# Kernel tuning notes

Measured on AMD Instinct MI355X. Metric: run time of the kernel, lower is better.

## Reference

```python
import jax, jax.numpy as jnp
from jax import lax
import numpy as np

K = 4            # prototypes per class: 3 kmeans centroids + 1 backbone
EPS = 0.1        # sinkhorn entropic regularization
MAX_ITER = 100
THRESH = 0.01
KM_ITERS = 10    # Lloyd iterations (replaces host-side sklearn KMeans)
HW = 28          # the original reshapes pred to 28x28, fixing n = 784


def setup_inputs():
    key = jax.random.key(0)
    k1, k2, k3, k4 = jax.random.split(key, 4)
    b, n, d, c = 32, HW * HW, 1024, 20
    return {
        "query": jax.random.normal(k1, (b, n, d), dtype=jnp.float32),
        "score": jax.random.uniform(k2, (b, n, c), dtype=jnp.float32),
        "label": jax.random.randint(k3, (b, c), 0, 2),
        "gt": jax.random.randint(k4, (b, HW, HW), 0, c + 1),
        "weights": jnp.array([1.0, 1.0, 0.0, -1.0], dtype=jnp.float32),
    }


def _assign(dq, cen, selfm):
    # dq [b,m,d], cen [b,c,j,d], selfm [b,c,m] float mask -> one-hot labels, counts
    x2 = jnp.sum(dq * dq, axis=-1)                                   # [b,m]
    d2 = (x2[:, None, :, None]
          - 2.0 * jnp.einsum('bmd,bcjd->bcmj', dq, cen)
          + jnp.sum(cen * cen, axis=-1)[:, :, None, :])              # [b,c,m,j]
    oh = jax.nn.one_hot(jnp.argmin(d2, axis=-1), cen.shape[2], dtype=dq.dtype) * selfm[..., None]
    return oh, oh.sum(axis=2)


def _sinkhorn(Km, u, v):
    # vectorized over the [b,c] pair grid, per-pair early exit as in the torch loop
    def cond(st):
        it, r, cc, done = st
        return (it < MAX_ITER) & jnp.logical_not(jnp.all(done))

    def body(st):
        it, r, cc, done = st
        r1 = u / jnp.einsum('bcnj,bcj->bcn', Km, cc)
        c1 = v / jnp.einsum('bcnj,bcn->bcj', Km, r1)
        err = jnp.mean(jnp.abs(r1 - r), axis=-1)                     # [b,c]
        r = jnp.where(done[..., None], r, r1)
        cc = jnp.where(done[..., None], cc, c1)
        done = done | (err < THRESH)
        return it + 1, r, cc, done

    st = (jnp.int32(0), jnp.ones_like(u), jnp.ones_like(v),
          jnp.zeros(Km.shape[:2], dtype=bool))
    _, r, cc, _ = lax.while_loop(cond, body, st)
    return r[..., :, None] * cc[..., None, :] * Km                   # [b,c,n,K]


def _forward(query, score, label, gt, weights):
    b, n, d = query.shape
    c = score.shape[2]
    dq, ds = query[:, ::2, :], score[:, ::2, :]                      # stride-2 downsample
    m = dq.shape[1]
    cls_assign = jnp.argmax(ds, axis=-1)                             # [b,m]
    sel = cls_assign[:, None, :] == jnp.arange(c)[None, :, None]     # [b,c,m]
    selfm = sel.astype(query.dtype)
    cnt = selfm.sum(-1)                                              # [b,c]
    valid = (label > 0) & (cnt >= K)

    # ---- masked Lloyd's k-means with k-1 = 3 clusters per (image, class) pair
    order = jnp.argsort((~sel).astype(jnp.int32), axis=-1)           # masked points first
    init_idx = order[..., :K - 1]                                    # [b,c,3]
    cen = dq[jnp.arange(b)[:, None, None], init_idx]                 # [b,c,3,d]

    def km_step(cen, _):
        oh, kcnt = _assign(dq, cen, selfm)
        sums = jnp.einsum('bmd,bcmj->bcjd', dq, oh)
        cen = jnp.where(kcnt[..., None] > 0,
                        sums / jnp.maximum(kcnt, 1.0)[..., None], cen)
        return cen, None

    cen, _ = lax.scan(km_step, cen, None, length=KM_ITERS)
    oh, kcnt = _assign(dq, cen, selfm)                               # final labels

    # ---- sort centroids by mean cluster score (descending)
    sm = ds.mean(axis=-1)                                            # [b,m]
    avg = jnp.where(kcnt > 0,
                    jnp.einsum('bm,bcmj->bcj', sm, oh) / jnp.maximum(kcnt, 1.0),
                    -jnp.inf)
    ordj = jnp.argsort(-avg, axis=-1)                                # [b,c,3]
    cen = jnp.take_along_axis(cen, ordj[..., None], axis=2)

    # ---- backbone prototype = mean over unselected downsampled tokens
    un = 1.0 - selfm
    backbone = jnp.einsum('bmd,bcm->bcd', dq, un) / jnp.maximum(m - cnt, 1.0)[..., None]
    protos = jnp.concatenate([cen, backbone[:, :, None, :]], axis=2)  # [b,c,4,d]

    # ---- OT between query[0] tokens and the 4 prototypes (original uses query[0] always)
    q0 = query[0]
    q0h = q0 / jnp.maximum(jnp.linalg.norm(q0, axis=-1, keepdims=True), 1e-12)
    ph = protos / jnp.maximum(jnp.linalg.norm(protos, axis=-1, keepdims=True), 1e-12)
    sim = jnp.einsum('nd,bcjd->bcnj', q0h, ph)                       # [b,c,n,4]
    Km = lax.stop_gradient(jnp.exp(-(1.0 - sim) / EPS))              # torch.no_grad
    u = jnp.full((b, c, n), 1.0 / n, dtype=query.dtype)
    v = jnp.full((b, c, K), 1.0 / K, dtype=query.dtype)
    T = lax.stop_gradient(_sinkhorn(Km, u, v))                       # [b,c,n,4]

    valid = valid & jnp.logical_not(jnp.any(jnp.isnan(T), axis=(2, 3)))
    pred = jnp.einsum('bcnj,j->bcn', T, weights)                     # [b,c,n]

    # ---- BCE vs gt masks (28x28 -> 28x28 bilinear resize is the identity)
    y = (gt.reshape(b, -1)[:, None, :] == (jnp.arange(c) + 1)[None, :, None]).astype(pred.dtype)
    p = jnp.clip(pred, 0.0, 1.0)
    bce = -(y * jnp.maximum(jnp.log(p), -100.0)
            + (1.0 - y) * jnp.maximum(jnp.log(1.0 - p), -100.0)).mean(axis=-1)  # [b,c]
    bce = jnp.where(valid, bce, 0.0)
    total_n = valid.sum().astype(pred.dtype)
    return bce.sum() / (total_n + 1e-4)


def reference(query, score, label, gt, weights):
    return _forward(query, score, label, gt, weights)
```

## Files before the change

kernel.cpp:

```cpp
#include <hip/hip_runtime.h>
#include <cmath>

#define BB 32
#define NN 784
#define MM 392
#define DD 1024
#define CC 20
#define JJ 3
#define KP 4
#define KM_ITERS 10
#define GMAX 64
#define NCOL (BB * CC * KP)
#define NQ0B 98
#define NTSB (BB * 16)

typedef __attribute__((ext_vector_type(8))) short bf16x8;
typedef __attribute__((ext_vector_type(4))) float f32x4;

__device__ inline unsigned short f2bf(float x) {
  unsigned int u = __float_as_uint(x);
  u += 0x7FFFu + ((u >> 16) & 1u);
  return (unsigned short)(u >> 16);
}
__device__ inline float bf2f(unsigned short h) {
  return __uint_as_float(((unsigned int)h) << 16);
}
__device__ inline void f2bf2(float x, unsigned short& hi, unsigned short& lo) {
  hi = f2bf(x);
  lo = f2bf(x - bf2f(hi));
}
__device__ inline void store_bf4(unsigned short* baseh, unsigned short* basel,
                                 int idx4, float4 v) {
  ushort4 h, l;
  f2bf2(v.x, h.x, l.x); f2bf2(v.y, h.y, l.y);
  f2bf2(v.z, h.z, l.z); f2bf2(v.w, h.w, l.w);
  ((ushort4*)baseh)[idx4] = h;
  ((ushort4*)basel)[idx4] = l;
}

__global__ __launch_bounds__(512) void k_prep(
    const float* __restrict__ score, const float* __restrict__ query,
    const int* __restrict__ label,
    int* __restrict__ cls, float* __restrict__ sm, int* __restrict__ valid,
    float* __restrict__ totalsum,
    unsigned short* __restrict__ q0hh, unsigned short* __restrict__ q0hl,
    float* __restrict__ gred) {
  int blk = blockIdx.x;
  int tid = threadIdx.x, lane = tid & 63, wv = tid >> 6;
  __shared__ int s_cnt[CC];
  __shared__ float sa[8][64];

  if (blk < BB) {
    int b = blk;
    if (tid < CC) s_cnt[tid] = 0;
    __syncthreads();
    if (tid < MM) {
      const float4* s4 = (const float4*)(score + ((size_t)b * NN + 2 * tid) * CC);
      float4 r[5];
      #pragma unroll
      for (int k = 0; k < 5; k++) r[k] = s4[k];
      const float* s = (const float*)r;
      float best = s[0]; int bi = 0; float acc = s[0];
      #pragma unroll
      for (int c = 1; c < CC; c++) { float v = s[c]; acc += v; if (v > best) { best = v; bi = c; } }
      cls[b * MM + tid] = bi;
      sm[b * MM + tid] = acc / (float)CC;
      atomicAdd(&s_cnt[bi], 1);
    }
    __syncthreads();
    if (tid < CC) {
      int cv = s_cnt[tid];
      valid[b * CC + tid] = (label[b * CC + tid] > 0 && cv >= KP) ? 1 : 0;
    }
    if (blk == 0 && tid == 0) { gred[0] = 0.f; gred[1] = 0.f; ((int*)gred)[2] = 0; }
  } else if (blk < BB + NQ0B) {
    int n = (blk - BB) * 8 + wv;
    const float* src = query + (size_t)n * DD;
    float v[16];
    float ss = 0.f;
    #pragma unroll
    for (int j = 0; j < 16; j++) { v[j] = src[lane + 64 * j]; ss += v[j] * v[j]; }
    #pragma unroll
    for (int o = 32; o > 0; o >>= 1) ss += __shfl_xor(ss, o, 64);
    float nrm = fmaxf(sqrtf(ss), 1e-12f);
    #pragma unroll
    for (int j = 0; j < 16; j++) {
      unsigned short hi, lo;
      f2bf2(v[j] / nrm, hi, lo);
      q0hh[(size_t)n * DD + lane + 64 * j] = hi;
      q0hl[(size_t)n * DD + lane + 64 * j] = lo;
    }
  } else {
    int t = blk - BB - NQ0B;
    int b = t >> 4, ch = t & 15;
    const float* qb = query + (size_t)b * NN * DD + ch * 64 + lane;
    float a = 0.f;
    #pragma unroll 7
    for (int r = 0; r < 49; r++) {
      int i = wv * 49 + r;
      a += qb[(size_t)(2 * i) * DD];
    }
    sa[wv][lane] = a;
    __syncthreads();
    if (wv == 0) {
      float s = 0.f;
      #pragma unroll
      for (int w = 0; w < 8; w++) s += sa[w][lane];
      totalsum[(size_t)b * DD + ch * 64 + lane] = s;
    }
  }
}

__global__ __launch_bounds__(512) void k_gram(
    const float* __restrict__ query, const int* __restrict__ cls,
    const int* __restrict__ valid, const float* __restrict__ sm,
    const float* __restrict__ totalsum,
    unsigned short* __restrict__ phh, unsigned short* __restrict__ phl) {
  int bc = blockIdx.x;
  if (!valid[bc]) return;
  int b = bc / CC, c = bc - b * CC;
  int tid = threadIdx.x, lane = tid & 63, wv = tid >> 6;
  const float* qb = query + (size_t)b * NN * DD;
  __shared__ int s_wtot[8];
  __shared__ int s_list[GMAX];
  __shared__ __align__(16) float Xs[GMAX][132];
  __shared__ float Gl[GMAX][65];
  __shared__ float s_w[JJ][GMAX];
  __shared__ int s_rank[JJ];
  __shared__ float s_red2[8];

  int flag = 0;
  if (tid < MM) flag = (cls[b * MM + tid] == c) ? 1 : 0;
  unsigned long long msk = __ballot(flag);
  int wp = __popcll(msk & ((1ull << lane) - 1ull));
  if (lane == 0) s_wtot[wv] = __popcll(msk);
  __syncthreads();
  int off = 0, mtot = 0;
  #pragma unroll
  for (int w = 0; w < 8; w++) { int t = s_wtot[w]; if (w < wv) off += t; mtot += t; }
  int mc = mtot > GMAX ? GMAX : mtot;
  if (flag) { int pos = off + wp; if (pos < GMAX) s_list[pos] = tid; }
  __syncthreads();

  const float* pb[4] = {nullptr, nullptr, nullptr, nullptr};
  float* xd[4] = {nullptr, nullptr, nullptr, nullptr};
  #pragma unroll
  for (int s = 0; s < 4; s++) {
    int e = tid + s * 512;
    if (e < mc * 32) {
      pb[s] = qb + (size_t)(2 * s_list[e >> 5]) * DD + (e & 31) * 4;
      xd[s] = &Xs[e >> 5][(e & 31) * 4];
    }
  }

  int T = (mc + 3) >> 2;
  int ntile = T * (T + 1) / 2;
  int ti = -1, tj = 0;
  float a[4][4] = {};
  if (tid < ntile) {
    int p = tid;
    int i = (int)floorf((sqrtf(8.0f * (float)p + 1.0f) - 1.0f) * 0.5f);
    while ((i + 1) * (i + 2) / 2 <= p) i++;
    while (i * (i + 1) / 2 > p) i--;
    ti = i; tj = p - i * (i + 1) / 2;
  }

  float4 cur[4], nxt[4];
  #pragma unroll
  for (int s = 0; s < 4; s++) {
    cur[s] = make_float4(0.f, 0.f, 0.f, 0.f);
    nxt[s] = make_float4(0.f, 0.f, 0.f, 0.f);
    if (pb[s]) cur[s] = *(const float4*)(pb[s]);
  }
  for (int ch = 0; ch < 8; ch++) {
    __syncthreads();
    #pragma unroll
    for (int s = 0; s < 4; s++) if (pb[s]) *(float4*)xd[s] = cur[s];
    if (ch < 7) {
      #pragma unroll
      for (int s = 0; s < 4; s++) if (pb[s]) nxt[s] = *(const float4*)(pb[s] + (ch + 1) * 128);
    }
    __syncthreads();
    if (ti >= 0) {
      const float4* xr0 = (const float4*)&Xs[4 * ti + 0][0];
      const float4* xr1 = (const float4*)&Xs[4 * ti + 1][0];
      const float4* xr2 = (const float4*)&Xs[4 * ti + 2][0];
      const float4* xr3 = (const float4*)&Xs[4 * ti + 3][0];
      const float4* xc0 = (const float4*)&Xs[4 * tj + 0][0];
      const float4* xc1 = (const float4*)&Xs[4 * tj + 1][0];
      const float4* xc2 = (const float4*)&Xs[4 * tj + 2][0];
      const float4* xc3 = (const float4*)&Xs[4 * tj + 3][0];
      #pragma unroll 8
      for (int kk = 0; kk < 32; kk++) {
        float4 u[4], w[4];
        u[0] = xr0[kk]; u[1] = xr1[kk]; u[2] = xr2[kk]; u[3] = xr3[kk];
        w[0] = xc0[kk]; w[1] = xc1[kk]; w[2] = xc2[kk]; w[3] = xc3[kk];
        #pragma unroll
        for (int r = 0; r < 4; r++)
          #pragma unroll
          for (int cq = 0; cq < 4; cq++)
            a[r][cq] += u[r].x * w[cq].x + u[r].y * w[cq].y
                      + u[r].z * w[cq].z + u[r].w * w[cq].w;
      }
    }
    #pragma unroll
    for (int s = 0; s < 4; s++) cur[s] = nxt[s];
  }

  if (ti >= 0) {
    #pragma unroll
    for (int r = 0; r < 4; r++) {
      int gr = 4 * ti + r;
      if (gr < mc) {
        #pragma unroll
        for (int cq = 0; cq < 4; cq++) {
          int gc = 4 * tj + cq;
          if (gc < mc) { Gl[gr][gc] = a[r][cq]; Gl[gc][gr] = a[r][cq]; }
        }
      }
    }
  }
  __syncthreads();

  if (wv == 0) {
    bool act = lane < mc;
    float smv = act ? sm[b * MM + s_list[lane]] : 0.f;
    s_w[0][lane] = (lane == 0) ? 1.f : 0.f;
    s_w[1][lane] = (lane == 1) ? 1.f : 0.f;
    s_w[2][lane] = (lane == 2) ? 1.f : 0.f;
    int aj = 0, n0 = 0, n1 = 0, n2 = 0;
    for (int it = 0; it <= KM_ITERS; it++) {
      float h0 = 0.f, h1 = 0.f, h2 = 0.f;
      if (act) {
        for (int i = 0; i < mc; i++) {
          float g = Gl[lane][i];
          h0 += s_w[0][i] * g; h1 += s_w[1][i] * g; h2 += s_w[2][i] * g;
        }
      }
      float t0 = s_w[0][lane] * h0, t1 = s_w[1][lane] * h1, t2 = s_w[2][lane] * h2;
      for (int o = 1; o < 64; o <<= 1) {
        t0 += __shfl_xor(t0, o, 64); t1 += __shfl_xor(t1, o, 64); t2 += __shfl_xor(t2, o, 64);
      }
      float e0 = t0 - 2.f * h0, e1 = t1 - 2.f * h1, e2 = t2 - 2.f * h2;
      aj = 0; float bv = e0;
      if (e1 < bv) { bv = e1; aj = 1; }
      if (e2 < bv) { bv = e2; aj = 2; }
      n0 = __popcll(__ballot(act && aj == 0));
      n1 = __popcll(__ballot(act && aj == 1));
      n2 = __popcll(__ballot(act && aj == 2));
      if (it == KM_ITERS) break;
      if (act) {
        if (n0 > 0) s_w[0][lane] = (aj == 0) ? 1.f / (float)n0 : 0.f;
        if (n1 > 0) s_w[1][lane] = (aj == 1) ? 1.f / (float)n1 : 0.f;
        if (n2 > 0) s_w[2][lane] = (aj == 2) ? 1.f / (float)n2 : 0.f;
      }
    }
    float s0 = (act && aj == 0) ? smv : 0.f;
    float s1 = (act && aj == 1) ? smv : 0.f;
    float s2 = (act && aj == 2) ? smv : 0.f;
    for (int o = 1; o < 64; o <<= 1) {
      s0 += __shfl_xor(s0, o, 64); s1 += __shfl_xor(s1, o, 64); s2 += __shfl_xor(s2, o, 64);
    }
    if (lane == 0) {
      float avg[JJ];
      avg[0] = (n0 > 0) ? s0 / (float)n0 : -INFINITY;
      avg[1] = (n1 > 0) ? s1 / (float)n1 : -INFINITY;
      avg[2] = (n2 > 0) ? s2 / (float)n2 : -INFINITY;
      bool used[JJ] = {false, false, false};
      for (int s = 0; s < JJ; s++) {
        int bi = -1; float bv = 0.f;
        for (int j = 0; j < JJ; j++)
          if (!used[j] && (bi < 0 || avg[j] > bv)) { bi = j; bv = avg[j]; }
        used[bi] = true; s_rank[bi] = s;
      }
    }
  }
  __syncthreads();

  float4 a0 = make_float4(0.f, 0.f, 0.f, 0.f), a1 = make_float4(0.f, 0.f, 0.f, 0.f);
  int j = tid >> 7, q = tid & 127;
  if (j < 3) {
    for (int g = 0; g < mc; g++) {
      float w = s_w[j][g];
      if (w != 0.f) {
        const float4* row = (const float4*)(qb + (size_t)(2 * s_list[g]) * DD);
        float4 v0 = row[q], v1 = row[q + 128];
        a0.x += w * v0.x; a0.y += w * v0.y; a0.z += w * v0.z; a0.w += w * v0.w;
        a1.x += w * v1.x; a1.y += w * v1.y; a1.z += w * v1.z; a1.w += w * v1.w;
      }
    }
  } else {
    for (int g = 0; g < mc; g++) {
      const float4* row = (const float4*)(qb + (size_t)(2 * s_list[g]) * DD);
      float4 v0 = row[q], v1 = row[q + 128];
      a0.x += v0.x; a0.y += v0.y; a0.z += v0.z; a0.w += v0.w;
      a1.x += v1.x; a1.y += v1.y; a1.z += v1.z; a1.w += v1.w;
    }
    const float4* tb = (const float4*)(totalsum + (size_t)b * DD);
    float4 t0 = tb[q], t1 = tb[q + 128];
    float denom = fmaxf((float)(MM - mtot), 1.f);
    float inv = 1.f / denom;
    a0.x = (t0.x - a0.x) * inv; a0.y = (t0.y - a0.y) * inv;
    a0.z = (t0.z - a0.z) * inv; a0.w = (t0.w - a0.w) * inv;
    a1.x = (t1.x - a1.x) * inv; a1.y = (t1.y - a1.y) * inv;
    a1.z = (t1.z - a1.z) * inv; a1.w = (t1.w - a1.w) * inv;
  }
  float ssq = a0.x * a0.x + a0.y * a0.y + a0.z * a0.z + a0.w * a0.w
            + a1.x * a1.x + a1.y * a1.y + a1.z * a1.z + a1.w * a1.w;
  #pragma unroll
  for (int o = 1; o < 64; o <<= 1) ssq += __shfl_xor(ssq, o, 64);
  if (lane == 0) s_red2[wv] = ssq;
  __syncthreads();
  float nrm = fmaxf(sqrtf(s_red2[2 * j] + s_red2[2 * j + 1]), 1e-12f);
  int prow = (j < 3) ? s_rank[j] : 3;
  size_t rowoff = ((size_t)bc * KP + prow) * DD;
  float4 o0 = make_float4(a0.x / nrm, a0.y / nrm, a0.z / nrm, a0.w / nrm);
  float4 o1 = make_float4(a1.x / nrm, a1.y / nrm, a1.z / nrm, a1.w / nrm);
  store_bf4(phh + rowoff, phl + rowoff, q, o0);
  store_bf4(phh + rowoff, phl + rowoff, q + 128, o1);
}

__global__ __launch_bounds__(64) void k_gemm(
    const unsigned short* __restrict__ Ah, const unsigned short* __restrict__ Al,
    const unsigned short* __restrict__ Bh, const unsigned short* __restrict__ Bl,
    float* __restrict__ P) {
  int n0 = blockIdx.y * 64;
  int m0 = blockIdx.x * 64;
  int lane = threadIdx.x;
  int kh = lane >> 4;
  int lr = lane & 15;

  const unsigned short* pa_h[4]; const unsigned short* pa_l[4];
  #pragma unroll
  for (int mi = 0; mi < 4; mi++) {
    size_t o = (size_t)(m0 + mi * 16 + lr) * DD + kh * 8;
    pa_h[mi] = Ah + o; pa_l[mi] = Al + o;
  }
  const unsigned short* pb_h[4]; const unsigned short* pb_l[4];
  #pragma unroll
  for (int ni = 0; ni < 4; ni++) {
    int col = n0 + ni * 16 + lr;
    size_t o = (size_t)col * DD + kh * 8;
    pb_h[ni] = Bh + o; pb_l[ni] = Bl + o;
  }

  f32x4 acc[4][4];
  #pragma unroll
  for (int mi = 0; mi < 4; mi++)
    #pragma unroll
    for (int ni = 0; ni < 4; ni++) acc[mi][ni] = (f32x4){0.f, 0.f, 0.f, 0.f};

  for (int k0 = 0; k0 < DD; k0 += 32) {
    bf16x8 ah[4], al[4], bh[4], bl[4];
    #pragma unroll
    for (int i = 0; i < 4; i++) {
      ah[i] = *(const bf16x8*)(pa_h[i] + k0);
      al[i] = *(const bf16x8*)(pa_l[i] + k0);
      bh[i] = *(const bf16x8*)(pb_h[i] + k0);
      bl[i] = *(const bf16x8*)(pb_l[i] + k0);
    }
    #pragma unroll
    for (int mi = 0; mi < 4; mi++)
      #pragma unroll
      for (int ni = 0; ni < 4; ni++) {
        acc[mi][ni] = __builtin_amdgcn_mfma_f32_16x16x32_bf16(ah[mi], bh[ni], acc[mi][ni], 0, 0, 0);
        acc[mi][ni] = __builtin_amdgcn_mfma_f32_16x16x32_bf16(ah[mi], bl[ni], acc[mi][ni], 0, 0, 0);
        acc[mi][ni] = __builtin_amdgcn_mfma_f32_16x16x32_bf16(al[mi], bh[ni], acc[mi][ni], 0, 0, 0);
      }
  }

  #pragma unroll
  for (int ni = 0; ni < 4; ni++) {
    int col = n0 + ni * 16 + lr;
    #pragma unroll
    for (int mi = 0; mi < 4; mi++) {
      int m = m0 + mi * 16 + kh * 4;
      if (m < NN) {
        *(f32x4*)(P + (size_t)col * NN + m) = acc[mi][ni];
      }
    }
  }
}

__global__ __launch_bounds__(256) void k_sink(const float* __restrict__ P,
    const int* __restrict__ valid, const int* __restrict__ gt,
    const float* __restrict__ wts, float* __restrict__ gred, float* __restrict__ out) {
  int wv = threadIdx.x >> 6, lane = threadIdx.x & 63;
  int bc = blockIdx.x * 4 + wv;
  int b = bc / CC, c = bc - b * CC;
  float bce_out = 0.f; int vld_out = 0;

  if (valid[bc]) {
    float4 kv[13]; float rr[13];
    #pragma unroll
    for (int s = 0; s < 13; s++) {
      int n = lane + 64 * s;
      kv[s] = make_float4(0.f, 0.f, 0.f, 0.f); rr[s] = 1.f;
      if (n < NN) {
        float4 o;
        o.x = expf(-(1.0f - P[((size_t)(4 * bc + 0)) * NN + n]) / 0.1f);
        o.y = expf(-(1.0f - P[((size_t)(4 * bc + 1)) * NN + n]) / 0.1f);
        o.z = expf(-(1.0f - P[((size_t)(4 * bc + 2)) * NN + n]) / 0.1f);
        o.w = expf(-(1.0f - P[((size_t)(4 * bc + 3)) * NN + n]) / 0.1f);
        kv[s] = o;
      }
    }
    const float uu = 1.0f / (float)NN, vv = 1.0f / (float)KP;
    float c0 = 1.f, c1 = 1.f, c2 = 1.f, c3 = 1.f;
    for (int it = 0; it < 100; it++) {
      float dsum = 0.f, p0 = 0.f, p1 = 0.f, p2 = 0.f, p3 = 0.f;
      #pragma unroll
      for (int s = 0; s < 13; s++) {
        int n = lane + 64 * s;
        if (n < NN) {
          float4 k4 = kv[s];
          float S = k4.x * c0 + k4.y * c1 + k4.z * c2 + k4.w * c3;
          float r1 = uu / S;
          dsum += fabsf(r1 - rr[s]);
          rr[s] = r1;
          p0 += k4.x * r1; p1 += k4.y * r1; p2 += k4.z * r1; p3 += k4.w * r1;
        }
      }
      #pragma unroll
      for (int o = 1; o < 64; o <<= 1) {
        dsum += __shfl_xor(dsum, o, 64);
        p0 += __shfl_xor(p0, o, 64); p1 += __shfl_xor(p1, o, 64);
        p2 += __shfl_xor(p2, o, 64); p3 += __shfl_xor(p3, o, 64);
      }
      c0 = vv / p0; c1 = vv / p1; c2 = vv / p2; c3 = vv / p3;
      if (dsum / (float)NN < 0.01f) break;
    }
    float w0 = wts[0], w1 = wts[1], w2 = wts[2], w3 = wts[3];
    float bsum = 0.f; int nanloc = 0;
    const int* gtb = gt + b * NN;
    #pragma unroll
    for (int s = 0; s < 13; s++) {
      int n = lane + 64 * s;
      if (n < NN) {
        float4 k4 = kv[s];
        float rv = rr[s];
        float T0 = rv * c0 * k4.x, T1 = rv * c1 * k4.y, T2 = rv * c2 * k4.z, T3 = rv * c3 * k4.w;
        if (T0 != T0 || T1 != T1 || T2 != T2 || T3 != T3) nanloc = 1;
        float pred = T0 * w0 + T1 * w1 + T2 * w2 + T3 * w3;
        float pcl = fminf(fmaxf(pred, 0.f), 1.f);
        float t = (gtb[n] == c + 1) ? fmaxf(logf(pcl), -100.f) : fmaxf(logf(1.f - pcl), -100.f);
        bsum += t;
      }
    }
    #pragma unroll
    for (int o = 1; o < 64; o <<= 1) bsum += __shfl_xor(bsum, o, 64);
    int nanany = __any(nanloc);
    if (!nanany) { bce_out = -(bsum / (float)NN); vld_out = 1; }
  }

  if (lane == 0) {
    if (vld_out) { atomicAdd(&gred[0], bce_out); atomicAdd(&gred[1], 1.f); }
    __threadfence();
    int old = atomicAdd((int*)gred + 2, 1);
    if (old == BB * CC - 1) {
      float s = atomicAdd(&gred[0], 0.f);
      float n2 = atomicAdd(&gred[1], 0.f);
      out[0] = s / (n2 + 0.0001f);
    }
  }
}

extern "C" void kernel_launch(void* const* d_in, const int* in_sizes, int n_in,
                              void* d_out, int out_size, void* d_ws, size_t ws_size,
                              hipStream_t stream) {
  (void)in_sizes; (void)n_in; (void)out_size; (void)ws_size;
  const float* query = (const float*)d_in[0];
  const float* score = (const float*)d_in[1];
  const int*   label = (const int*)d_in[2];
  const int*   gt    = (const int*)d_in[3];
  const float* wts   = (const float*)d_in[4];
  float* ws = (float*)d_ws;

  size_t off = 0;
  int* cls = (int*)(ws + off);            off += (size_t)BB * MM;
  float* sm = ws + off;                   off += (size_t)BB * MM;
  int* valid = (int*)(ws + off);          off += (size_t)BB * CC;
  float* totalsum = ws + off;             off += (size_t)BB * DD;
  unsigned short* q0hh = (unsigned short*)(ws + off);  off += (size_t)NN * DD / 2;
  unsigned short* q0hl = (unsigned short*)(ws + off);  off += (size_t)NN * DD / 2;
  unsigned short* phh = (unsigned short*)(ws + off);   off += (size_t)BB * CC * KP * DD / 2;
  unsigned short* phl = (unsigned short*)(ws + off);   off += (size_t)BB * CC * KP * DD / 2;
  float* P = ws + off;                    off += (size_t)NCOL * NN;
  float* gred = ws + off;                 off += 16;

  k_prep<<<BB + NQ0B + NTSB, 512, 0, stream>>>(score, query, label, cls, sm, valid,
                                               totalsum, q0hh, q0hl, gred);
  k_gram<<<BB * CC, 512, 0, stream>>>(query, cls, valid, sm, totalsum, phh, phl);
  dim3 gg((NN + 63) / 64, NCOL / 64);
  k_gemm<<<gg, 64, 0, stream>>>(q0hh, q0hl, phh, phl, P);
  k_sink<<<160, 256, 0, stream>>>(P, valid, gt, wts, gred, (float*)d_out);
}
```

Before: 309.8 us.

## Fuse similarity GEMM into Sinkhorn kernel and retile Gram computation to 2x2

Merges the bf16-split MFMA similarity GEMM into the Sinkhorn kernel. Each 256-thread block computes its 16 prototype columns over all 784 query rows into shared memory, then runs Sinkhorn straight from LDS, which removes the global P buffer round trip and one kernel launch. Separately, the Gram kernel switches from 4x4 to 2x2 register tiles with up to two tiles per thread, trading register pressure for more parallel tiles. The fused GEMM uses single 16x16 MFMA tiles per wave with no operand reuse across tiles, so it reloads the query operand from global memory in every block.

```diff
diff --git a/kernel.cpp b/kernel.cpp
--- a/kernel.cpp
+++ b/kernel.cpp
@@ -153,16 +153,21 @@
     }
   }
 
-  int T = (mc + 3) >> 2;
+  int T = (mc + 1) >> 1;
   int ntile = T * (T + 1) / 2;
-  int ti = -1, tj = 0;
-  float a[4][4] = {};
-  if (tid < ntile) {
-    int p = tid;
-    int i = (int)floorf((sqrtf(8.0f * (float)p + 1.0f) - 1.0f) * 0.5f);
-    while ((i + 1) * (i + 2) / 2 <= p) i++;
-    while (i * (i + 1) / 2 > p) i--;
-    ti = i; tj = p - i * (i + 1) / 2;
+  int ti_[2], tj_[2];
+  float a00[2], a01[2], a10[2], a11[2];
+  #pragma unroll
+  for (int s = 0; s < 2; s++) {
+    ti_[s] = -1; tj_[s] = 0;
+    a00[s] = 0.f; a01[s] = 0.f; a10[s] = 0.f; a11[s] = 0.f;
+    int p = tid + s * 512;
+    if (p < ntile) {
+      int i = (int)floorf((sqrtf(8.0f * (float)p + 1.0f) - 1.0f) * 0.5f);
+      while ((i + 1) * (i + 2) / 2 <= p) i++;
+      while (i * (i + 1) / 2 > p) i--;
+      ti_[s] = i; tj_[s] = p - i * (i + 1) / 2;
+    }
   }
 
   float4 cur[4], nxt[4];
@@ -181,43 +186,37 @@
       for (int s = 0; s < 4; s++) if (pb[s]) nxt[s] = *(const float4*)(pb[s] + (ch + 1) * 128);
     }
     __syncthreads();
-    if (ti >= 0) {
-      const float4* xr0 = (const float4*)&Xs[4 * ti + 0][0];
-      const float4* xr1 = (const float4*)&Xs[4 * ti + 1][0];
-      const float4* xr2 = (const float4*)&Xs[4 * ti + 2][0];
-      const float4* xr3 = (const float4*)&Xs[4 * ti + 3][0];
-      const float4* xc0 = (const float4*)&Xs[4 * tj + 0][0];
-      const float4* xc1 = (const float4*)&Xs[4 * tj + 1][0];
-      const float4* xc2 = (const float4*)&Xs[4 * tj + 2][0];
-      const float4* xc3 = (const float4*)&Xs[4 * tj + 3][0];
-      #pragma unroll 8
-      for (int kk = 0; kk < 32; kk++) {
-        float4 u[4], w[4];
-        u[0] = xr0[kk]; u[1] = xr1[kk]; u[2] = xr2[kk]; u[3] = xr3[kk];
-        w[0] = xc0[kk]; w[1] = xc1[kk]; w[2] = xc2[kk]; w[3] = xc3[kk];
+    #pragma unroll
+    for (int s = 0; s < 2; s++) {
+      if (ti_[s] >= 0) {
+        const float4* xr0 = (const float4*)&Xs[2 * ti_[s]][0];
+        const float4* xr1 = (const float4*)&Xs[2 * ti_[s] + 1][0];
+        const float4* xc0 = (const float4*)&Xs[2 * tj_[s]][0];
+        const float4* xc1 = (const float4*)&Xs[2 * tj_[s] + 1][0];
+        float s00 = 0.f, s01 = 0.f, s10 = 0.f, s11 = 0.f;
         #pragma unroll
-        for (int r = 0; r < 4; r++)
-          #pragma unroll
-          for (int cq = 0; cq < 4; cq++)
-            a[r][cq] += u[r].x * w[cq].x + u[r].y * w[cq].y
-                      + u[r].z * w[cq].z + u[r].w * w[cq].w;
+        for (int kk = 0; kk < 32; kk++) {
+          float4 u0 = xr0[kk], u1 = xr1[kk], w0 = xc0[kk], w1 = xc1[kk];
+          s00 += u0.x * w0.x + u0.y * w0.y + u0.z * w0.z + u0.w * w0.w;
+          s01 += u0.x * w1.x + u0.y * w1.y + u0.z * w1.z + u0.w * w1.w;
+          s10 += u1.x * w0.x + u1.y * w0.y + u1.z * w0.z + u1.w * w0.w;
+          s11 += u1.x * w1.x + u1.y * w1.y + u1.z * w1.z + u1.w * w1.w;
+        }
+        a00[s] += s00; a01[s] += s01; a10[s] += s10; a11[s] += s11;
       }
     }
     #pragma unroll
     for (int s = 0; s < 4; s++) cur[s] = nxt[s];
   }
 
-  if (ti >= 0) {
-    #pragma unroll
-    for (int r = 0; r < 4; r++) {
-      int gr = 4 * ti + r;
-      if (gr < mc) {
-        #pragma unroll
-        for (int cq = 0; cq < 4; cq++) {
-          int gc = 4 * tj + cq;
-          if (gc < mc) { Gl[gr][gc] = a[r][cq]; Gl[gc][gr] = a[r][cq]; }
-        }
-      }
+  #pragma unroll
+  for (int s = 0; s < 2; s++) {
+    if (ti_[s] >= 0) {
+      int r0 = 2 * ti_[s], r1 = r0 + 1, c0 = 2 * tj_[s], c1 = c0 + 1;
+      if (r0 < mc && c0 < mc) { Gl[r0][c0] = a00[s]; Gl[c0][r0] = a00[s]; }
+      if (r0 < mc && c1 < mc) { Gl[r0][c1] = a01[s]; Gl[c1][r0] = a01[s]; }
+      if (r1 < mc && c0 < mc) { Gl[r1][c0] = a10[s]; Gl[c0][r1] = a10[s]; }
+      if (r1 < mc && c1 < mc) { Gl[r1][c1] = a11[s]; Gl[c1][r1] = a11[s]; }
     }
   }
   __syncthreads();
@@ -320,72 +319,37 @@
   store_bf4(phh + rowoff, phl + rowoff, q + 128, o1);
 }
 
-__global__ __launch_bounds__(64) void k_gemm(
+__global__ __launch_bounds__(256) void k_gs(
     const unsigned short* __restrict__ Ah, const unsigned short* __restrict__ Al,
     const unsigned short* __restrict__ Bh, const unsigned short* __restrict__ Bl,
-    float* __restrict__ P) {
-  int n0 = blockIdx.y * 64;
-  int m0 = blockIdx.x * 64;
-  int lane = threadIdx.x;
-  int kh = lane >> 4;
-  int lr = lane & 15;
-
-  const unsigned short* pa_h[4]; const unsigned short* pa_l[4];
-  #pragma unroll
-  for (int mi = 0; mi < 4; mi++) {
-    size_t o = (size_t)(m0 + mi * 16 + lr) * DD + kh * 8;
-    pa_h[mi] = Ah + o; pa_l[mi] = Al + o;
-  }
-  const unsigned short* pb_h[4]; const unsigned short* pb_l[4];
-  #pragma unroll
-  for (int ni = 0; ni < 4; ni++) {
-    int col = n0 + ni * 16 + lr;
-    size_t o = (size_t)col * DD + kh * 8;
-    pb_h[ni] = Bh + o; pb_l[ni] = Bl + o;
-  }
-
-  f32x4 acc[4][4];
-  #pragma unroll
-  for (int mi = 0; mi < 4; mi++)
-    #pragma unroll
-    for (int ni = 0; ni < 4; ni++) acc[mi][ni] = (f32x4){0.f, 0.f, 0.f, 0.f};
-
-  for (int k0 = 0; k0 < DD; k0 += 32) {
-    bf16x8 ah[4], al[4], bh[4], bl[4];
-    #pragma unroll
-    for (int i = 0; i < 4; i++) {
-      ah[i] = *(const bf16x8*)(pa_h[i] + k0);
-      al[i] = *(const bf16x8*)(pa_l[i] + k0);
-      bh[i] = *(const bf16x8*)(pb_h[i] + k0);
-      bl[i] = *(const bf16x8*)(pb_l[i] + k0);
-    }
-    #pragma unroll
-    for (int mi = 0; mi < 4; mi++)
-      #pragma unroll
-      for (int ni = 0; ni < 4; ni++) {
-        acc[mi][ni] = __builtin_amdgcn_mfma_f32_16x16x32_bf16(ah[mi], bh[ni], acc[mi][ni], 0, 0, 0);
-        acc[mi][ni] = __builtin_amdgcn_mfma_f32_16x16x32_bf16(ah[mi], bl[ni], acc[mi][ni], 0, 0, 0);
-        acc[mi][ni] = __builtin_amdgcn_mfma_f32_16x16x32_bf16(al[mi], bh[ni], acc[mi][ni], 0, 0, 0);
-      }
-  }
-
-  #pragma unroll
-  for (int ni = 0; ni < 4; ni++) {
-    int col = n0 + ni * 16 + lr;
-    #pragma unroll
-    for (int mi = 0; mi < 4; mi++) {
-      int m = m0 + mi * 16 + kh * 4;
-      if (m < NN) {
-        *(f32x4*)(P + (size_t)col * NN + m) = acc[mi][ni];
-      }
-    }
-  }
-}
-
-__global__ __launch_bounds__(256) void k_sink(const float* __restrict__ P,
     const int* __restrict__ valid, const int* __restrict__ gt,
     const float* __restrict__ wts, float* __restrict__ gred, float* __restrict__ out) {
-  int wv = threadIdx.x >> 6, lane = threadIdx.x & 63;
+  __shared__ float s_P[NN][17];
+  int tid = threadIdx.x, lane = tid & 63, wv = tid >> 6;
+  int col0 = blockIdx.x * 16;
+  int lr = lane & 15, kh = lane >> 4;
+
+  const unsigned short* pbh = Bh + (size_t)(col0 + lr) * DD + kh * 8;
+  const unsigned short* pbl = Bl + (size_t)(col0 + lr) * DD + kh * 8;
+  for (int mt = wv; mt < 49; mt += 4) {
+    const unsigned short* pah = Ah + (size_t)(mt * 16 + lr) * DD + kh * 8;
+    const unsigned short* pal = Al + (size_t)(mt * 16 + lr) * DD + kh * 8;
+    f32x4 acc = (f32x4){0.f, 0.f, 0.f, 0.f};
+    for (int k0 = 0; k0 < DD; k0 += 32) {
+      bf16x8 fah = *(const bf16x8*)(pah + k0);
+      bf16x8 fal = *(const bf16x8*)(pal + k0);
+      bf16x8 fbh = *(const bf16x8*)(pbh + k0);
+      bf16x8 fbl = *(const bf16x8*)(pbl + k0);
+      acc = __builtin_amdgcn_mfma_f32_16x16x32_bf16(fah, fbh, acc, 0, 0, 0);
+      acc = __builtin_amdgcn_mfma_f32_16x16x32_bf16(fah, fbl, acc, 0, 0, 0);
+      acc = __builtin_amdgcn_mfma_f32_16x16x32_bf16(fal, fbh, acc, 0, 0, 0);
+    }
+    #pragma unroll
+    for (int r = 0; r < 4; r++)
+      s_P[mt * 16 + kh * 4 + r][lr] = acc[r];
+  }
+  __syncthreads();
+
   int bc = blockIdx.x * 4 + wv;
   int b = bc / CC, c = bc - b * CC;
   float bce_out = 0.f; int vld_out = 0;
@@ -397,11 +361,12 @@
       int n = lane + 64 * s;
       kv[s] = make_float4(0.f, 0.f, 0.f, 0.f); rr[s] = 1.f;
       if (n < NN) {
+        int cb = (wv << 2);
         float4 o;
-        o.x = expf(-(1.0f - P[((size_t)(4 * bc + 0)) * NN + n]) / 0.1f);
-        o.y = expf(-(1.0f - P[((size_t)(4 * bc + 1)) * NN + n]) / 0.1f);
-        o.z = expf(-(1.0f - P[((size_t)(4 * bc + 2)) * NN + n]) / 0.1f);
-        o.w = expf(-(1.0f - P[((size_t)(4 * bc + 3)) * NN + n]) / 0.1f);
+        o.x = expf(-(1.0f - s_P[n][cb + 0]) / 0.1f);
+        o.y = expf(-(1.0f - s_P[n][cb + 1]) / 0.1f);
+        o.z = expf(-(1.0f - s_P[n][cb + 2]) / 0.1f);
+        o.w = expf(-(1.0f - s_P[n][cb + 3]) / 0.1f);
         kv[s] = o;
       }
     }
@@ -485,13 +450,11 @@
   unsigned short* q0hl = (unsigned short*)(ws + off);  off += (size_t)NN * DD / 2;
   unsigned short* phh = (unsigned short*)(ws + off);   off += (size_t)BB * CC * KP * DD / 2;
   unsigned short* phl = (unsigned short*)(ws + off);   off += (size_t)BB * CC * KP * DD / 2;
-  float* P = ws + off;                    off += (size_t)NCOL * NN;
   float* gred = ws + off;                 off += 16;
 
   k_prep<<<BB + NQ0B + NTSB, 512, 0, stream>>>(score, query, label, cls, sm, valid,
                                                totalsum, q0hh, q0hl, gred);
   k_gram<<<BB * CC, 512, 0, stream>>>(query, cls, valid, sm, totalsum, phh, phl);
-  dim3 gg((NN + 63) / 64, NCOL / 64);
-  k_gemm<<<gg, 64, 0, stream>>>(q0hh, q0hl, phh, phl, P);
-  k_sink<<<160, 256, 0, stream>>>(P, valid, gt, wts, gred, (float*)d_out);
-}
+  k_gs<<<NCOL / 16, 256, 0, stream>>>(q0hh, q0hl, phh, phl, valid, gt, wts, gred,
+                                      (float*)d_out);
+}
```

New measurement: 387.8 us. 25.2% more time.

## Compute k_gram Gram matrix with bf16x3 MFMA and one-wave sink blocks

Applied to the files above, without the earlier changes.

The Gram matrix of up to 64 selected rows in k_gram was computed with scalar FP32 FMAs over LDS-staged 4x4 tiles. It now uses 16x16 MFMA tiles, one wave per tile and up to two tiles per wave. Each tile reads global rows directly and splits them into bf16 hi/lo pairs, using three MFMAs per k-step to keep close to FP32 accuracy, with a zeroed buffer padding out-of-range rows. The weighted-sum loop also drops its zero-weight branch, and k_sink launches one 64-thread block per (b,c) pair instead of four waves per block. The MFMA path removes the shared-memory staging and scalar FMA cost, but rereads rows from global/L2 for each tile and does extra conversion work.

```diff
diff --git a/kernel.cpp b/kernel.cpp
--- a/kernel.cpp
+++ b/kernel.cpp
@@ -37,6 +37,17 @@
   ((ushort4*)baseh)[idx4] = h;
   ((ushort4*)basel)[idx4] = l;
 }
+__device__ inline void cvt8(const float4& x0, const float4& x1, bf16x8& h8, bf16x8& l8) {
+  float xs[8] = {x0.x, x0.y, x0.z, x0.w, x1.x, x1.y, x1.z, x1.w};
+  bf16x8 h, l;
+  #pragma unroll
+  for (int i = 0; i < 8; i++) {
+    unsigned short hi, lo;
+    f2bf2(xs[i], hi, lo);
+    h[i] = (short)hi; l[i] = (short)lo;
+  }
+  h8 = h; l8 = l;
+}
 
 __global__ __launch_bounds__(512) void k_prep(
     const float* __restrict__ score, const float* __restrict__ query,
@@ -44,7 +55,7 @@
     int* __restrict__ cls, float* __restrict__ sm, int* __restrict__ valid,
     float* __restrict__ totalsum,
     unsigned short* __restrict__ q0hh, unsigned short* __restrict__ q0hl,
-    float* __restrict__ gred) {
+    float* __restrict__ gred, float* __restrict__ zbuf) {
   int blk = blockIdx.x;
   int tid = threadIdx.x, lane = tid & 63, wv = tid >> 6;
   __shared__ int s_cnt[CC];
@@ -72,7 +83,10 @@
       int cv = s_cnt[tid];
       valid[b * CC + tid] = (label[b * CC + tid] > 0 && cv >= KP) ? 1 : 0;
     }
-    if (blk == 0 && tid == 0) { gred[0] = 0.f; gred[1] = 0.f; ((int*)gred)[2] = 0; }
+    if (blk == 0) {
+      if (tid == 0) { gred[0] = 0.f; gred[1] = 0.f; ((int*)gred)[2] = 0; }
+      zbuf[tid] = 0.f; zbuf[tid + 512] = 0.f;
+    }
   } else if (blk < BB + NQ0B) {
     int n = (blk - BB) * 8 + wv;
     const float* src = query + (size_t)n * DD;
@@ -114,7 +128,7 @@
 __global__ __launch_bounds__(512) void k_gram(
     const float* __restrict__ query, const int* __restrict__ cls,
     const int* __restrict__ valid, const float* __restrict__ sm,
-    const float* __restrict__ totalsum,
+    const float* __restrict__ totalsum, const float* __restrict__ zbuf,
     unsigned short* __restrict__ phh, unsigned short* __restrict__ phl) {
   int bc = blockIdx.x;
   if (!valid[bc]) return;
@@ -123,7 +137,6 @@
   const float* qb = query + (size_t)b * NN * DD;
   __shared__ int s_wtot[8];
   __shared__ int s_list[GMAX];
-  __shared__ __align__(16) float Xs[GMAX][132];
   __shared__ float Gl[GMAX][65];
   __shared__ float s_w[JJ][GMAX];
   __shared__ int s_rank[JJ];
@@ -142,81 +155,54 @@
   if (flag) { int pos = off + wp; if (pos < GMAX) s_list[pos] = tid; }
   __syncthreads();
 
-  const float* pb[4] = {nullptr, nullptr, nullptr, nullptr};
-  float* xd[4] = {nullptr, nullptr, nullptr, nullptr};
-  #pragma unroll
-  for (int s = 0; s < 4; s++) {
-    int e = tid + s * 512;
-    if (e < mc * 32) {
-      pb[s] = qb + (size_t)(2 * s_list[e >> 5]) * DD + (e & 31) * 4;
-      xd[s] = &Xs[e >> 5][(e & 31) * 4];
-    }
-  }
-
-  int T = (mc + 3) >> 2;
-  int ntile = T * (T + 1) / 2;
-  int ti = -1, tj = 0;
-  float a[4][4] = {};
-  if (tid < ntile) {
-    int p = tid;
-    int i = (int)floorf((sqrtf(8.0f * (float)p + 1.0f) - 1.0f) * 0.5f);
-    while ((i + 1) * (i + 2) / 2 <= p) i++;
-    while (i * (i + 1) / 2 > p) i--;
-    ti = i; tj = p - i * (i + 1) / 2;
-  }
-
-  float4 cur[4], nxt[4];
-  #pragma unroll
-  for (int s = 0; s < 4; s++) {
-    cur[s] = make_float4(0.f, 0.f, 0.f, 0.f);
-    nxt[s] = make_float4(0.f, 0.f, 0.f, 0.f);
-    if (pb[s]) cur[s] = *(const float4*)(pb[s]);
-  }
-  for (int ch = 0; ch < 8; ch++) {
-    __syncthreads();
-    #pragma unroll
-    for (int s = 0; s < 4; s++) if (pb[s]) *(float4*)xd[s] = cur[s];
-    if (ch < 7) {
-      #pragma unroll
-      for (int s = 0; s < 4; s++) if (pb[s]) nxt[s] = *(const float4*)(pb[s] + (ch + 1) * 128);
-    }
-    __syncthreads();
-    if (ti >= 0) {
-      const float4* xr0 = (const float4*)&Xs[4 * ti + 0][0];
-      const float4* xr1 = (const float4*)&Xs[4 * ti + 1][0];
-      const float4* xr2 = (const float4*)&Xs[4 * ti + 2][0];
-      const float4* xr3 = (const float4*)&Xs[4 * ti + 3][0];
-      const float4* xc0 = (const float4*)&Xs[4 * tj + 0][0];
-      const float4* xc1 = (const float4*)&Xs[4 * tj + 1][0];
-      const float4* xc2 = (const float4*)&Xs[4 * tj + 2][0];
-      const float4* xc3 = (const float4*)&Xs[4 * tj + 3][0];
-      #pragma unroll 8
-      for (int kk = 0; kk < 32; kk++) {
-        float4 u[4], w[4];
-        u[0] = xr0[kk]; u[1] = xr1[kk]; u[2] = xr2[kk]; u[3] = xr3[kk];
-        w[0] = xc0[kk]; w[1] = xc1[kk]; w[2] = xc2[kk]; w[3] = xc3[kk];
-        #pragma unroll
-        for (int r = 0; r < 4; r++)
-          #pragma unroll
-          for (int cq = 0; cq < 4; cq++)
-            a[r][cq] += u[r].x * w[cq].x + u[r].y * w[cq].y
-                      + u[r].z * w[cq].z + u[r].w * w[cq].w;
-      }
-    }
-    #pragma unroll
-    for (int s = 0; s < 4; s++) cur[s] = nxt[s];
-  }
-
-  if (ti >= 0) {
-    #pragma unroll
-    for (int r = 0; r < 4; r++) {
-      int gr = 4 * ti + r;
-      if (gr < mc) {
-        #pragma unroll
-        for (int cq = 0; cq < 4; cq++) {
-          int gc = 4 * tj + cq;
-          if (gc < mc) { Gl[gr][gc] = a[r][cq]; Gl[gc][gr] = a[r][cq]; }
-        }
+  int T16 = (mc + 15) >> 4;
+  int ntile16 = T16 * (T16 + 1) / 2;
+  int fr = lane & 15, fkq = lane >> 4;
+
+  int tis[2], tjs[2];
+  const float* pA[2]; const float* pB[2];
+  f32x4 accs[2];
+  #pragma unroll
+  for (int tt = 0; tt < 2; tt++) {
+    accs[tt] = (f32x4){0.f, 0.f, 0.f, 0.f};
+    tis[tt] = -1; tjs[tt] = 0; pA[tt] = zbuf; pB[tt] = zbuf;
+    int t = wv + 8 * tt;
+    if (t < ntile16) {
+      int i = 0;
+      while ((i + 1) * (i + 2) / 2 <= t) i++;
+      tis[tt] = i; tjs[tt] = t - i * (i + 1) / 2;
+      int ra = 16 * tis[tt] + fr, rb = 16 * tjs[tt] + fr;
+      pA[tt] = (ra < mc) ? qb + (size_t)(2 * s_list[ra]) * DD + fkq * 8 : zbuf + fkq * 8;
+      pB[tt] = (rb < mc) ? qb + (size_t)(2 * s_list[rb]) * DD + fkq * 8 : zbuf + fkq * 8;
+    }
+  }
+
+  for (int ks = 0; ks < 32; ks++) {
+    #pragma unroll
+    for (int tt = 0; tt < 2; tt++) {
+      if (tis[tt] >= 0) {
+        float4 a0 = *(const float4*)(pA[tt] + 32 * ks);
+        float4 a1 = *(const float4*)(pA[tt] + 32 * ks + 4);
+        float4 b0 = *(const float4*)(pB[tt] + 32 * ks);
+        float4 b1 = *(const float4*)(pB[tt] + 32 * ks + 4);
+        bf16x8 ah, al, bh, bl;
+        cvt8(a0, a1, ah, al);
+        cvt8(b0, b1, bh, bl);
+        accs[tt] = __builtin_amdgcn_mfma_f32_16x16x32_bf16(ah, bh, accs[tt], 0, 0, 0);
+        accs[tt] = __builtin_amdgcn_mfma_f32_16x16x32_bf16(ah, bl, accs[tt], 0, 0, 0);
+        accs[tt] = __builtin_amdgcn_mfma_f32_16x16x32_bf16(al, bh, accs[tt], 0, 0, 0);
+      }
+    }
+  }
+
+  #pragma unroll
+  for (int tt = 0; tt < 2; tt++) {
+    if (tis[tt] >= 0) {
+      #pragma unroll
+      for (int r = 0; r < 4; r++) {
+        int gr = 16 * tis[tt] + fkq * 4 + r;
+        int gc = 16 * tjs[tt] + fr;
+        Gl[gr][gc] = accs[tt][r]; Gl[gc][gr] = accs[tt][r];
       }
     }
   }
@@ -282,12 +268,10 @@
   if (j < 3) {
     for (int g = 0; g < mc; g++) {
       float w = s_w[j][g];
-      if (w != 0.f) {
-        const float4* row = (const float4*)(qb + (size_t)(2 * s_list[g]) * DD);
-        float4 v0 = row[q], v1 = row[q + 128];
-        a0.x += w * v0.x; a0.y += w * v0.y; a0.z += w * v0.z; a0.w += w * v0.w;
-        a1.x += w * v1.x; a1.y += w * v1.y; a1.z += w * v1.z; a1.w += w * v1.w;
-      }
+      const float4* row = (const float4*)(qb + (size_t)(2 * s_list[g]) * DD);
+      float4 v0 = row[q], v1 = row[q + 128];
+      a0.x += w * v0.x; a0.y += w * v0.y; a0.z += w * v0.z; a0.w += w * v0.w;
+      a1.x += w * v1.x; a1.y += w * v1.y; a1.z += w * v1.z; a1.w += w * v1.w;
     }
   } else {
     for (int g = 0; g < mc; g++) {
@@ -382,11 +366,11 @@
   }
 }
 
-__global__ __launch_bounds__(256) void k_sink(const float* __restrict__ P,
+__global__ __launch_bounds__(64) void k_sink(const float* __restrict__ P,
     const int* __restrict__ valid, const int* __restrict__ gt,
     const float* __restrict__ wts, float* __restrict__ gred, float* __restrict__ out) {
-  int wv = threadIdx.x >> 6, lane = threadIdx.x & 63;
-  int bc = blockIdx.x * 4 + wv;
+  int lane = threadIdx.x;
+  int bc = blockIdx.x;
   int b = bc / CC, c = bc - b * CC;
   float bce_out = 0.f; int vld_out = 0;
 
@@ -487,11 +471,12 @@
   unsigned short* phl = (unsigned short*)(ws + off);   off += (size_t)BB * CC * KP * DD / 2;
   float* P = ws + off;                    off += (size_t)NCOL * NN;
   float* gred = ws + off;                 off += 16;
+  float* zbuf = ws + off;                 off += 1024;
 
   k_prep<<<BB + NQ0B + NTSB, 512, 0, stream>>>(score, query, label, cls, sm, valid,
-                                               totalsum, q0hh, q0hl, gred);
-  k_gram<<<BB * CC, 512, 0, stream>>>(query, cls, valid, sm, totalsum, phh, phl);
+                                               totalsum, q0hh, q0hl, gred, zbuf);
+  k_gram<<<BB * CC, 512, 0, stream>>>(query, cls, valid, sm, totalsum, zbuf, phh, phl);
   dim3 gg((NN + 63) / 64, NCOL / 64);
   k_gemm<<<gg, 64, 0, stream>>>(q0hh, q0hl, phh, phl, P);
-  k_sink<<<160, 256, 0, stream>>>(P, valid, gt, wts, gred, (float*)d_out);
-}
+  k_sink<<<BB * CC, 64, 0, stream>>>(P, valid, gt, wts, gred, (float*)d_out);
+}
```

After: 283.1 us. -8.6%, faster.
